# Kernel tuning notes

Hardware: AMD Instinct MI355X
Metric: run time of the kernel (lower is better)

Reference implementation:

```python
import jax, jax.numpy as jnp
from jax import lax
import numpy as np

B, DIM, H, W = 4, 64, 256, 256
HEADS = 8
# (pad_h, pad_w) for kernels (1,7),(1,11),(1,21),(7,1),(11,1),(21,1)
PADS = [(0, 3), (0, 5), (0, 10), (3, 0), (5, 0), (10, 0)]
KSHAPES = [(1, 7), (1, 11), (1, 21), (7, 1), (11, 1), (21, 1)]


def _ln(x, w, b):
    # LayerNorm over channel dim per pixel (torch does it in 'b (h w) c' layout)
    mu = jnp.mean(x, axis=1, keepdims=True)
    var = jnp.mean((x - mu) ** 2, axis=1, keepdims=True)  # unbiased=False
    return (x - mu) / jnp.sqrt(var + 1e-5) * w[None, :, None, None] + b[None, :, None, None]


def _dw(x, k, b, pad):
    # depthwise conv, k: (dim, 1, kh, kw)
    y = lax.conv_general_dilated(
        x, k, window_strides=(1, 1),
        padding=[(pad[0], pad[0]), (pad[1], pad[1])],
        feature_group_count=k.shape[0],
        dimension_numbers=('NCHW', 'OIHW', 'NCHW'))
    return y + b[None, :, None, None]


def _pw(x, w, b):
    # 1x1 conv
    return jnp.einsum('oc,bchw->bohw', w, x) + b[None, :, None, None]


def _l2n(x):
    # torch F.normalize(dim=-1): x / max(||x||_2, 1e-12)
    n = jnp.sqrt(jnp.sum(x * x, axis=-1, keepdims=True))
    return x / jnp.maximum(n, 1e-12)


def _to_attn(t, b, h, w, cph):
    # 'b (head c) h w -> b head w (h c)'  (h slow, c fast in last dim)
    t = t.reshape(b, HEADS, cph, h, w)
    return t.transpose(0, 1, 4, 3, 2).reshape(b, HEADS, w, h * cph)


def setup_inputs() -> dict:
    key = jax.random.key(0)
    keys = jax.random.split(key, 16)
    inp = {
        'x1': jax.random.normal(keys[0], (B, DIM, H, W), jnp.float32),
        'x2': jax.random.normal(keys[1], (B, DIM, H, W), jnp.float32),
        'ln1_w': jnp.ones((DIM,), jnp.float32),
        'ln1_b': jnp.zeros((DIM,), jnp.float32),
        'ln2_w': jnp.ones((DIM,), jnp.float32),
        'ln2_b': jnp.zeros((DIM,), jnp.float32),
        'b_dw': jnp.zeros((12, DIM), jnp.float32),
        'w_pw': 0.05 * jax.random.normal(keys[2], (DIM, DIM), jnp.float32),
        'b_pw': jnp.zeros((DIM,), jnp.float32),
    }
    names = ['k11', 'k12', 'k13', 'k14', 'k15', 'k16',
             'k21', 'k22', 'k23', 'k24', 'k25', 'k26']
    for i, nm in enumerate(names):
        kh, kw = KSHAPES[i % 6]
        inp[nm] = 0.1 * jax.random.normal(keys[3 + i], (DIM, 1, kh, kw), jnp.float32)
    return inp


def reference(x1, x2, ln1_w, ln1_b, ln2_w, ln2_b,
              k11, k12, k13, k14, k15, k16,
              k21, k22, k23, k24, k25, k26,
              b_dw, w_pw, b_pw):
    b, c, h, w = x2.shape
    cph = c // HEADS
    x1n = _ln(x1, ln1_w, ln1_b)
    x2n = _ln(x2, ln2_w, ln2_b)
    ks1 = (k11, k12, k13, k14, k15, k16)
    ks2 = (k21, k22, k23, k24, k25, k26)
    out1 = sum(_dw(x1n, k, b_dw[i], PADS[i]) for i, k in enumerate(ks1))
    out2 = sum(_dw(x2n, k, b_dw[6 + i], PADS[i]) for i, k in enumerate(ks2))
    out1 = _pw(out1, w_pw, b_pw)  # shared 1x1 conv (same weights for both)
    out2 = _pw(out2, w_pw, b_pw)
    q = _l2n(_to_attn(out1, b, h, w, cph))   # (b, head, w, h*cph)
    kk = _l2n(_to_attn(out2, b, h, w, cph))
    v = _to_attn(out2, b, h, w, cph)
    attn = jax.nn.softmax(jnp.einsum('bnwd,bnvd->bnwv', q, kk), axis=-1)
    out4 = jnp.einsum('bnwv,bnvd->bnwd', attn, v) + q
    out4 = out4.reshape(b, HEADS, w, h, cph).transpose(0, 1, 4, 3, 2).reshape(b, c, h, w)
    # note: torch rebinds x1/x2 to normalized tensors before the residual add
    return _pw(out4, w_pw, b_pw) + x1n + x2n
```

## Files before the change

kernel.cpp:

```cpp
#include <hip/hip_runtime.h>

#define HW 65536

typedef __bf16 bf16x8 __attribute__((ext_vector_type(8)));
typedef float f32x4 __attribute__((ext_vector_type(4)));

__device__ __forceinline__ float b2f(unsigned short u) {
    return __uint_as_float(((unsigned)u) << 16);
}
__device__ __forceinline__ unsigned short f2bu(float f) {
    unsigned u = __float_as_uint(f);
    return (unsigned short)((u + 0x7FFFu + ((u >> 16) & 1u)) >> 16);
}
__device__ __forceinline__ void up2(unsigned u, float& lo, float& hi) {
    lo = __uint_as_float(u << 16);
    hi = __uint_as_float(u & 0xFFFF0000u);
}

__global__ void k_prep(const float* k11, const float* k12, const float* k13,
                       const float* k14, const float* k15, const float* k16,
                       const float* k21, const float* k22, const float* k23,
                       const float* k24, const float* k25, const float* k26,
                       const float* bdw, float* wcomb, float* bias) {
    int c = threadIdx.x;
    if (c >= 64) return;
    float* wh1 = wcomb;
    float* wv1 = wcomb + 1344;
    float* wh2 = wcomb + 2688;
    float* wv2 = wcomb + 4032;
    for (int j = 0; j < 21; j++) {
        wh1[c*21+j] = k13[c*21+j];
        wv1[c*21+j] = k16[c*21+j];
        wh2[c*21+j] = k23[c*21+j];
        wv2[c*21+j] = k26[c*21+j];
    }
    for (int j = 0; j < 11; j++) {
        wh1[c*21+j+5] += k12[c*11+j];
        wv1[c*21+j+5] += k15[c*11+j];
        wh2[c*21+j+5] += k22[c*11+j];
        wv2[c*21+j+5] += k25[c*11+j];
    }
    for (int j = 0; j < 7; j++) {
        wh1[c*21+j+7] += k11[c*7+j];
        wv1[c*21+j+7] += k14[c*7+j];
        wh2[c*21+j+7] += k21[c*7+j];
        wv2[c*21+j+7] += k24[c*7+j];
    }
    float s1 = 0.f, s2 = 0.f;
    for (int i = 0; i < 6; i++) { s1 += bdw[i*64+c]; s2 += bdw[(6+i)*64+c]; }
    bias[c] = s1; bias[64+c] = s2;
}

__global__ __launch_bounds__(256) void k_ln(
        const float* __restrict__ x1, const float* __restrict__ x2,
        const float* __restrict__ w1, const float* __restrict__ b1,
        const float* __restrict__ w2, const float* __restrict__ b2,
        unsigned short* __restrict__ o1, unsigned short* __restrict__ o2,
        unsigned short* __restrict__ s12) {
    int p = blockIdx.x * 256 + threadIdx.x;
    int b = p >> 16, hw = p & (HW - 1);
    size_t base = (size_t)b * 64 * HW + hw;
    float v[64];
    unsigned n1[32];
    {
        float s = 0.f;
        #pragma unroll
        for (int c = 0; c < 64; c++) { v[c] = x1[base + (size_t)c * HW]; s += v[c]; }
        float mu = s * 0.015625f, s2 = 0.f;
        #pragma unroll
        for (int c = 0; c < 64; c++) { float d = v[c] - mu; s2 += d * d; }
        float rstd = rsqrtf(s2 * 0.015625f + 1e-5f);
        #pragma unroll
        for (int c2 = 0; c2 < 32; c2++) {
            unsigned short lo = f2bu((v[2*c2]   - mu) * rstd * w1[2*c2]   + b1[2*c2]);
            unsigned short hi = f2bu((v[2*c2+1] - mu) * rstd * w1[2*c2+1] + b1[2*c2+1]);
            o1[base + (size_t)(2*c2)   * HW] = lo;
            o1[base + (size_t)(2*c2+1) * HW] = hi;
            n1[c2] = (unsigned)lo | ((unsigned)hi << 16);
        }
    }
    {
        float s = 0.f;
        #pragma unroll
        for (int c = 0; c < 64; c++) { v[c] = x2[base + (size_t)c * HW]; s += v[c]; }
        float mu = s * 0.015625f, s2 = 0.f;
        #pragma unroll
        for (int c = 0; c < 64; c++) { float d = v[c] - mu; s2 += d * d; }
        float rstd = rsqrtf(s2 * 0.015625f + 1e-5f);
        #pragma unroll
        for (int c2 = 0; c2 < 32; c2++) {
            float a2 = (v[2*c2]   - mu) * rstd * w2[2*c2]   + b2[2*c2];
            float b2n = (v[2*c2+1] - mu) * rstd * w2[2*c2+1] + b2[2*c2+1];
            o2[base + (size_t)(2*c2)   * HW] = f2bu(a2);
            o2[base + (size_t)(2*c2+1) * HW] = f2bu(b2n);
            float lo, hi;
            up2(n1[c2], lo, hi);
            s12[base + (size_t)(2*c2)   * HW] = f2bu(lo + a2);
            s12[base + (size_t)(2*c2+1) * HW] = f2bu(hi + b2n);
        }
    }
}

__global__ __launch_bounds__(256) void k_dw(
        const unsigned short* __restrict__ in1, const unsigned short* __restrict__ in2,
        const float* __restrict__ wcomb, const float* __restrict__ bias,
        unsigned short* __restrict__ o1, unsigned short* __restrict__ o2) {
    __shared__ __align__(16) unsigned short tileRaw[52 * 320];
    __shared__ __align__(16) unsigned short ThT[16][64];
    __shared__ __align__(16) unsigned short TvA[16][64];
    int which = blockIdx.y;
    const unsigned short* in = which ? in2 : in1;
    unsigned short* o = which ? o2 : o1;
    int bx = blockIdx.x;
    int bc = bx >> 3, tileid = bx & 7;
    int c = bc & 63;
    int h0 = tileid * 32;
    int tid = threadIdx.x;

    {
        const float* whp = wcomb + which * 2688 + c * 21;
        const float* wvp = whp + 1344;
        for (int i = tid; i < 2048; i += 256) {
            int mat = i >> 10;
            int idx = i & 1023;
            int n = idx >> 6, k = idx & 63;
            int j = k - n - 6;
            float v = (j >= 0 && j < 21) ? (mat ? wvp[j] : whp[j]) : 0.f;
            (mat ? &TvA[0][0] : &ThT[0][0])[idx] = f2bu(v);
        }
    }
    const unsigned short* src = in + (size_t)bc * HW;
    for (int idx = tid; idx < 52 * 40; idx += 256) {
        int row = idx / 40, u = idx - row * 40;
        int grow = h0 - 10 + row;
        uint4 val = make_uint4(0u, 0u, 0u, 0u);
        if ((unsigned)grow < 256u && u >= 2 && u < 34)
            val = *(const uint4*)(src + grow * 256 + (u - 2) * 8);
        *(uint4*)&tileRaw[row * 320 + ((u ^ ((row >> 1) & 7)) << 3)] = val;
    }
    float bs = bias[which * 64 + c];
    __syncthreads();

    int lane = tid & 63, wid = tid >> 6;
    int rA = lane & 15, g = lane >> 4, kf = g * 8;

    bf16x8 thB0 = *(const bf16x8*)&ThT[rA][kf];
    bf16x8 thB1 = *(const bf16x8*)&ThT[rA][32 + kf];
    bf16x8 tvA0 = *(const bf16x8*)&TvA[rA][kf];
    bf16x8 tvA1 = *(const bf16x8*)&TvA[rA][32 + kf];

    int ht = wid & 1, wgrp = wid >> 1;
    for (int t = 0; t < 8; t++) {
        int w0 = (wgrp * 8 + t) * 16;
        int ub = w0 >> 3;
        int hrow = ht * 16 + rA + 10;
        int xh = (hrow >> 1) & 7;
        bf16x8 ax0 = *(const bf16x8*)&tileRaw[hrow * 320 + (((ub + g) ^ xh) << 3)];
        bf16x8 ax1 = *(const bf16x8*)&tileRaw[hrow * 320 + (((ub + 4 + g) ^ xh) << 3)];
        int uvb = ub + 2 + (rA >> 3);
        int el = rA & 7;
        uint4 bv0, bv1;
        unsigned* pv0 = (unsigned*)&bv0;
        unsigned* pv1 = (unsigned*)&bv1;
        #pragma unroll
        for (int e2 = 0; e2 < 4; e2++) {
            int k0i = kf + 2 * e2;
            int r0 = ht * 16 + k0i - 6;  r0 = r0 < 0 ? 0 : (r0 > 51 ? 51 : r0);
            int r1 = ht * 16 + k0i - 5;  r1 = r1 < 0 ? 0 : (r1 > 51 ? 51 : r1);
            unsigned lo = tileRaw[r0 * 320 + ((uvb ^ ((r0 >> 1) & 7)) << 3) + el];
            unsigned hi = tileRaw[r1 * 320 + ((uvb ^ ((r1 >> 1) & 7)) << 3) + el];
            pv0[e2] = lo | (hi << 16);
            int k1i = 32 + kf + 2 * e2;
            int r2 = ht * 16 + k1i - 6;  r2 = r2 < 0 ? 0 : (r2 > 51 ? 51 : r2);
            int r3 = ht * 16 + k1i - 5;  r3 = r3 < 0 ? 0 : (r3 > 51 ? 51 : r3);
            unsigned lo2 = tileRaw[r2 * 320 + ((uvb ^ ((r2 >> 1) & 7)) << 3) + el];
            unsigned hi2 = tileRaw[r3 * 320 + ((uvb ^ ((r3 >> 1) & 7)) << 3) + el];
            pv1[e2] = lo2 | (hi2 << 16);
        }
        f32x4 acc = {bs, bs, bs, bs};
        acc = __builtin_amdgcn_mfma_f32_16x16x32_bf16(ax0, thB0, acc, 0, 0, 0);
        acc = __builtin_amdgcn_mfma_f32_16x16x32_bf16(ax1, thB1, acc, 0, 0, 0);
        acc = __builtin_amdgcn_mfma_f32_16x16x32_bf16(tvA0, *(bf16x8*)&bv0, acc, 0, 0, 0);
        acc = __builtin_amdgcn_mfma_f32_16x16x32_bf16(tvA1, *(bf16x8*)&bv1, acc, 0, 0, 0);
        int wc = w0 + rA;
        size_t obase = (size_t)bc * HW + wc;
        #pragma unroll
        for (int r = 0; r < 4; r++) {
            int hh = h0 + ht * 16 + 4 * g + r;
            o[obase + (size_t)hh * 256] = f2bu(acc[r]);
        }
    }
}

__global__ __launch_bounds__(256) void k_pw(
        const unsigned short* __restrict__ in1, const unsigned short* __restrict__ in2,
        const float* __restrict__ wpw, const float* __restrict__ bpw,
        unsigned short* __restrict__ Eq, unsigned short* __restrict__ Fk,
        unsigned short* __restrict__ Fv) {
    __shared__ __align__(16) unsigned short Ws[64][72];
    __shared__ __align__(16) unsigned short Xs[64][260];
    __shared__ float sb[64];
    int tid = threadIdx.x;
    for (int i = tid; i < 4096; i += 256) Ws[i >> 6][i & 63] = f2bu(wpw[i]);
    if (tid < 64) sb[tid] = bpw[tid];
    int which = blockIdx.y;
    const unsigned short* in = which ? in2 : in1;
    int bx = blockIdx.x;
    int b = bx & 3;
    int h = ((bx >> 2) & 31) * 8 + (bx >> 7);
    const unsigned short* src = in + (size_t)b * 64 * HW + h * 256;
    for (int i = tid; i < 2048; i += 256) {
        int c = i >> 5, ch = i & 31;
        uint4 u = *(const uint4*)(src + (size_t)c * HW + ch * 8);
        *(uint2*)&Xs[c][ch * 8]     = make_uint2(u.x, u.y);
        *(uint2*)&Xs[c][ch * 8 + 4] = make_uint2(u.z, u.w);
    }
    __syncthreads();

    int lane = tid & 63, wv = tid >> 6;
    int rA = lane & 15, g = lane >> 4;
    int p_off = wv * 64;

    f32x4 acc[4][4];
    #pragma unroll
    for (int m = 0; m < 4; m++)
        #pragma unroll
        for (int n = 0; n < 4; n++) acc[m][n] = (f32x4){0.f, 0.f, 0.f, 0.f};

    #pragma unroll
    for (int ks = 0; ks < 2; ks++) {
        int c0 = ks * 32;
        bf16x8 a[4], bb[4];
        #pragma unroll
        for (int m = 0; m < 4; m++)
            a[m] = *(const bf16x8*)&Ws[16 * m + rA][c0 + 8 * g];
        #pragma unroll
        for (int n = 0; n < 4; n++) {
            int p = p_off + 16 * n + rA;
            uint4 bu;
            bu.x = (unsigned)Xs[c0 + 8*g + 0][p] | ((unsigned)Xs[c0 + 8*g + 1][p] << 16);
            bu.y = (unsigned)Xs[c0 + 8*g + 2][p] | ((unsigned)Xs[c0 + 8*g + 3][p] << 16);
            bu.z = (unsigned)Xs[c0 + 8*g + 4][p] | ((unsigned)Xs[c0 + 8*g + 5][p] << 16);
            bu.w = (unsigned)Xs[c0 + 8*g + 6][p] | ((unsigned)Xs[c0 + 8*g + 7][p] << 16);
            bb[n] = *(bf16x8*)&bu;
        }
        #pragma unroll
        for (int m = 0; m < 4; m++)
            #pragma unroll
            for (int n = 0; n < 4; n++)
                acc[m][n] = __builtin_amdgcn_mfma_f32_16x16x32_bf16(a[m], bb[n], acc[m][n], 0, 0, 0);
    }

    unsigned short* dst = which ? Fk : Eq;
    size_t b8 = (size_t)b * 8;
    #pragma unroll
    for (int m = 0; m < 4; m++) {
        int o0 = 16 * m + 4 * g;
        int hd = o0 >> 3, cp = o0 & 7;
        #pragma unroll
        for (int n = 0; n < 4; n++) {
            int p = p_off + 16 * n + rA;
            ushort4 pk;
            #pragma unroll
            for (int r = 0; r < 4; r++)
                ((unsigned short*)&pk)[r] = f2bu(acc[m][n][r] + sb[o0 + r]);
            *(ushort4*)(dst + ((b8 + hd) * 256 + p) * 2048 + h * 8 + cp) = pk;
            if (which) {
                #pragma unroll
                for (int r = 0; r < 4; r++) {
                    int o = o0 + r;
                    Fv[((b8 + (o >> 3)) * 2048 + h * 8 + (o & 7)) * 256 + p] =
                        ((unsigned short*)&pk)[r];
                }
            }
        }
    }
}

__global__ __launch_bounds__(256) void k_norm(
        const unsigned short* __restrict__ Eq, const unsigned short* __restrict__ Fk,
        float* __restrict__ invQ, float* __restrict__ invK) {
    int lane = threadIdx.x & 63, wid = threadIdx.x >> 6;
    int row = blockIdx.x * 4 + wid;
    const unsigned short* src = (row < 8192) ? Eq : Fk;
    int r = row & 8191;
    const unsigned short* p = src + (size_t)r * 2048;
    float s = 0.f;
    #pragma unroll
    for (int it = 0; it < 4; it++) {
        uint4 u = *(const uint4*)(p + it * 512 + lane * 8);
        unsigned vals[4] = {u.x, u.y, u.z, u.w};
        #pragma unroll
        for (int e = 0; e < 4; e++) {
            float lo = b2f((unsigned short)(vals[e] & 0xffffu));
            float hi = b2f((unsigned short)(vals[e] >> 16));
            s += lo * lo + hi * hi;
        }
    }
    #pragma unroll
    for (int m = 1; m < 64; m <<= 1) s += __shfl_xor(s, m, 64);
    if (lane == 0) {
        float inv = 1.f / fmaxf(sqrtf(s), 1e-12f);
        (row < 8192 ? invQ : invK)[r] = inv;
    }
}

__global__ __launch_bounds__(512, 4) void k_qkt(
        const unsigned short* __restrict__ Eq, const unsigned short* __restrict__ Fk,
        float* __restrict__ Sp) {
    int bx = blockIdx.x;
    int bh = bx & 31, t2 = bx >> 5;
    int itile = t2 >> 1, ks = t2 & 1;
    int i0 = itile * 32;
    const unsigned short* Q  = Eq + (size_t)bh * 524288 + ks * 1024;
    const unsigned short* Kp = Fk + (size_t)bh * 524288 + ks * 1024;
    int tid = threadIdx.x, lane = tid & 63, wid = tid >> 6;
    int rA = lane & 15, g = lane >> 4, kf = g * 8;

    f32x4 acc[2][2];
    #pragma unroll
    for (int ib = 0; ib < 2; ib++)
        #pragma unroll
        for (int jb = 0; jb < 2; jb++) acc[ib][jb] = (f32x4){0.f, 0.f, 0.f, 0.f};

    const unsigned short* q0  = Q  + (size_t)(i0 + rA) * 2048 + kf;
    const unsigned short* q1  = q0 + 16 * 2048;
    const unsigned short* kr0 = Kp + (size_t)(wid * 32 + rA) * 2048 + kf;
    const unsigned short* kr1 = kr0 + 16 * 2048;
    for (int k0 = 0; k0 < 1024; k0 += 128) {
        bf16x8 a0[4], a1[4], b0[4], b1[4];
        #pragma unroll
        for (int s = 0; s < 4; s++) {
            int kk = k0 + s * 32;
            a0[s] = *(const bf16x8*)(q0 + kk);
            a1[s] = *(const bf16x8*)(q1 + kk);
            b0[s] = *(const bf16x8*)(kr0 + kk);
            b1[s] = *(const bf16x8*)(kr1 + kk);
        }
        #pragma unroll
        for (int s = 0; s < 4; s++) {
            acc[0][0] = __builtin_amdgcn_mfma_f32_16x16x32_bf16(a0[s], b0[s], acc[0][0], 0, 0, 0);
            acc[1][0] = __builtin_amdgcn_mfma_f32_16x16x32_bf16(a1[s], b0[s], acc[1][0], 0, 0, 0);
            acc[0][1] = __builtin_amdgcn_mfma_f32_16x16x32_bf16(a0[s], b1[s], acc[0][1], 0, 0, 0);
            acc[1][1] = __builtin_amdgcn_mfma_f32_16x16x32_bf16(a1[s], b1[s], acc[1][1], 0, 0, 0);
        }
    }
    float* Sb = Sp + (size_t)(ks * 32 + bh) * 65536 + (size_t)i0 * 256;
    #pragma unroll
    for (int ib = 0; ib < 2; ib++)
        #pragma unroll
        for (int jb = 0; jb < 2; jb++)
            #pragma unroll
            for (int r = 0; r < 4; r++)
                Sb[(ib * 16 + g * 4 + r) * 256 + wid * 32 + jb * 16 + rA] = acc[ib][jb][r];
}

__global__ __launch_bounds__(256) void k_smx(
        const float* __restrict__ Sp, const float* __restrict__ invQ,
        const float* __restrict__ invK, unsigned short* __restrict__ P) {
    __shared__ float sKv[256];
    int bx = blockIdx.x;
    int bh = bx & 31, rg = bx >> 5;
    int tid = threadIdx.x;
    sKv[tid] = invK[bh * 256 + tid];
    __syncthreads();
    int lr = tid >> 5, sub = tid & 31;
    int i = rg * 8 + lr;
    int R = bh * 256 + i;
    const float* p0 = Sp + (size_t)bh * 65536 + i * 256;
    const float* p1 = Sp + (size_t)(32 + bh) * 65536 + i * 256;
    float qs = invQ[R];
    int c0 = sub * 8;
    float4 a0 = *(const float4*)(p0 + c0), a1 = *(const float4*)(p0 + c0 + 4);
    float4 b0 = *(const float4*)(p1 + c0), b1 = *(const float4*)(p1 + c0 + 4);
    float v[8];
    v[0] = (a0.x + b0.x); v[1] = (a0.y + b0.y); v[2] = (a0.z + b0.z); v[3] = (a0.w + b0.w);
    v[4] = (a1.x + b1.x); v[5] = (a1.y + b1.y); v[6] = (a1.z + b1.z); v[7] = (a1.w + b1.w);
    float m = -1e30f;
    #pragma unroll
    for (int e = 0; e < 8; e++) {
        v[e] *= qs * sKv[c0 + e];
        m = fmaxf(m, v[e]);
    }
    #pragma unroll
    for (int msk = 1; msk < 32; msk <<= 1) m = fmaxf(m, __shfl_xor(m, msk, 32));
    float s = 0.f;
    #pragma unroll
    for (int e = 0; e < 8; e++) { v[e] = __expf(v[e] - m); s += v[e]; }
    #pragma unroll
    for (int msk = 1; msk < 32; msk <<= 1) s += __shfl_xor(s, msk, 32);
    float inv = 1.f / s;
    uint4 w;
    w.x = (unsigned)f2bu(v[0] * inv) | ((unsigned)f2bu(v[1] * inv) << 16);
    w.y = (unsigned)f2bu(v[2] * inv) | ((unsigned)f2bu(v[3] * inv) << 16);
    w.z = (unsigned)f2bu(v[4] * inv) | ((unsigned)f2bu(v[5] * inv) << 16);
    w.w = (unsigned)f2bu(v[6] * inv) | ((unsigned)f2bu(v[7] * inv) << 16);
    *(uint4*)(P + (size_t)R * 256 + c0) = w;
}

__global__ __launch_bounds__(512, 4) void k_pv(
        const unsigned short* __restrict__ P, const unsigned short* __restrict__ Fv,
        const unsigned short* __restrict__ Eq, const float* __restrict__ invQ,
        unsigned short* __restrict__ G) {
    __shared__ __align__(16) unsigned short Pb[32][256];
    __shared__ __align__(16) unsigned short Qs[32][1024];
    __shared__ float sQ[32];
    int bx = blockIdx.x;
    int bh = bx & 31, t2 = bx >> 5;
    int itile = t2 >> 1, ds = t2 & 1;
    int i0 = itile * 32;
    int b = bh >> 3, hd = bh & 7;
    const unsigned short* Vt = Fv + (size_t)bh * 524288;
    int tid = threadIdx.x, lane = tid & 63, wid = tid >> 6;
    for (int i = tid; i < 1024; i += 512) {
        int r = i >> 5, cu = i & 31;
        uint4 u = *(const uint4*)(P + (size_t)(bh * 256 + i0 + r) * 256 + cu * 8);
        int su = cu ^ (r & 7);
        *(uint4*)&Pb[r][su * 8] = u;
    }
    for (int i = tid; i < 4096; i += 512) {
        int r = i >> 7, cu = i & 127;
        *(uint4*)&Qs[r][cu * 8] =
            *(const uint4*)(Eq + (size_t)(bh * 256 + i0 + r) * 2048 + ds * 1024 + cu * 8);
    }
    if (tid < 32) sQ[tid] = invQ[bh * 256 + i0 + tid];
    __syncthreads();

    int rA = lane & 15, g = lane >> 4, kf = g * 8;

    bf16x8 pa[2][8];
    #pragma unroll
    for (int ib = 0; ib < 2; ib++)
        #pragma unroll
        for (int ksl = 0; ksl < 8; ksl++) {
            int rr = ib * 16 + rA;
            int unit = (ksl * 4 + g) ^ (rr & 7);
            pa[ib][ksl] = *(const bf16x8*)&Pb[rr][unit * 8];
        }

    int dloc = wid * 128;
    for (int dt = 0; dt < 8; dt++) {
        int dl = dloc + dt * 16;
        int d0 = ds * 1024 + dl;
        const unsigned short* vp = Vt + (size_t)(d0 + rA) * 256 + kf;
        bf16x8 vb[8];
        #pragma unroll
        for (int ksl = 0; ksl < 8; ksl++)
            vb[ksl] = *(const bf16x8*)(vp + ksl * 32);
        f32x4 o0 = {0.f, 0.f, 0.f, 0.f}, o1 = {0.f, 0.f, 0.f, 0.f};
        #pragma unroll
        for (int ksl = 0; ksl < 8; ksl++) {
            o0 = __builtin_amdgcn_mfma_f32_16x16x32_bf16(pa[0][ksl], vb[ksl], o0, 0, 0, 0);
            o1 = __builtin_amdgcn_mfma_f32_16x16x32_bf16(pa[1][ksl], vb[ksl], o1, 0, 0, 0);
        }
        int d = d0 + rA;
        int dlr = dl + rA;
        int cpr = d & 7, hh = d >> 3;
        #pragma unroll
        for (int ib = 0; ib < 2; ib++) {
            f32x4 oa = ib ? o1 : o0;
            int ibase = i0 + ib * 16 + g * 4;
            ushort4 pk;
            #pragma unroll
            for (int r = 0; r < 4; r++) {
                int il = ib * 16 + g * 4 + r;
                float qv = b2f(Qs[il][dlr]) * sQ[il];
                ((unsigned short*)&pk)[r] = f2bu(oa[r] + qv);
            }
            *(ushort4*)(G + (size_t)(b * 64 + hd * 8 + cpr) * HW + hh * 256 + ibase) = pk;
        }
    }
}

__global__ __launch_bounds__(256) void k_final(
        const unsigned short* __restrict__ G, const unsigned short* __restrict__ S12g,
        const float* __restrict__ wpw, const float* __restrict__ bpw,
        float* __restrict__ out) {
    __shared__ __align__(16) unsigned short Ws[64][72];
    __shared__ __align__(16) unsigned short Gs[64][260];
    __shared__ __align__(16) unsigned short S12[64][260];
    __shared__ float sb[64];
    int tid = threadIdx.x;
    for (int i = tid; i < 4096; i += 256) Ws[i >> 6][i & 63] = f2bu(wpw[i]);
    if (tid < 64) sb[tid] = bpw[tid];
    int bx = blockIdx.x, b = bx >> 8, h = bx & 255;
    const unsigned short* src = G + (size_t)b * 64 * HW + h * 256;
    const unsigned short* ssrc = S12g + (size_t)b * 64 * HW + h * 256;
    for (int i = tid; i < 2048; i += 256) {
        int c = i >> 5, ch = i & 31;
        uint4 u = *(const uint4*)(src + (size_t)c * HW + ch * 8);
        *(uint2*)&Gs[c][ch * 8]     = make_uint2(u.x, u.y);
        *(uint2*)&Gs[c][ch * 8 + 4] = make_uint2(u.z, u.w);
        uint4 v = *(const uint4*)(ssrc + (size_t)c * HW + ch * 8);
        *(uint2*)&S12[c][ch * 8]     = make_uint2(v.x, v.y);
        *(uint2*)&S12[c][ch * 8 + 4] = make_uint2(v.z, v.w);
    }
    __syncthreads();

    int lane = tid & 63, wv = tid >> 6;
    int rA = lane & 15, g = lane >> 4;
    int p_off = wv * 64;

    f32x4 acc[4][4];
    #pragma unroll
    for (int m = 0; m < 4; m++)
        #pragma unroll
        for (int n = 0; n < 4; n++) acc[m][n] = (f32x4){0.f, 0.f, 0.f, 0.f};

    #pragma unroll
    for (int ks = 0; ks < 2; ks++) {
        int c0 = ks * 32;
        bf16x8 a[4], bb[4];
        #pragma unroll
        for (int m = 0; m < 4; m++)
            a[m] = *(const bf16x8*)&Ws[16 * m + rA][c0 + 8 * g];
        #pragma unroll
        for (int n = 0; n < 4; n++) {
            int p = p_off + 16 * n + rA;
            uint4 bu;
            bu.x = (unsigned)Gs[c0 + 8*g + 0][p] | ((unsigned)Gs[c0 + 8*g + 1][p] << 16);
            bu.y = (unsigned)Gs[c0 + 8*g + 2][p] | ((unsigned)Gs[c0 + 8*g + 3][p] << 16);
            bu.z = (unsigned)Gs[c0 + 8*g + 4][p] | ((unsigned)Gs[c0 + 8*g + 5][p] << 16);
            bu.w = (unsigned)Gs[c0 + 8*g + 6][p] | ((unsigned)Gs[c0 + 8*g + 7][p] << 16);
            bb[n] = *(bf16x8*)&bu;
        }
        #pragma unroll
        for (int m = 0; m < 4; m++)
            #pragma unroll
            for (int n = 0; n < 4; n++)
                acc[m][n] = __builtin_amdgcn_mfma_f32_16x16x32_bf16(a[m], bb[n], acc[m][n], 0, 0, 0);
    }

    #pragma unroll
    for (int m = 0; m < 4; m++) {
        int o0 = 16 * m + 4 * g;
        #pragma unroll
        for (int n = 0; n < 4; n++) {
            int p = p_off + 16 * n + rA;
            #pragma unroll
            for (int r = 0; r < 4; r++) {
                int o = o0 + r;
                out[(size_t)(b * 64 + o) * HW + h * 256 + p] =
                    acc[m][n][r] + sb[o] + b2f(S12[o][p]);
            }
        }
    }
}

extern "C" void kernel_launch(void* const* d_in, const int* in_sizes, int n_in,
                              void* d_out, int out_size, void* d_ws, size_t ws_size,
                              hipStream_t stream) {
    const float* x1   = (const float*)d_in[0];
    const float* x2   = (const float*)d_in[1];
    const float* ln1w = (const float*)d_in[2];
    const float* ln1b = (const float*)d_in[3];
    const float* ln2w = (const float*)d_in[4];
    const float* ln2b = (const float*)d_in[5];
    const float* bdw  = (const float*)d_in[6];
    const float* wpw  = (const float*)d_in[7];
    const float* bpw  = (const float*)d_in[8];
    const float* kk[12];
    for (int i = 0; i < 12; i++) kk[i] = (const float*)d_in[9 + i];

    char* ws = (char*)d_ws;
    float* wcomb = (float*)ws;
    float* bias  = (float*)(ws + 21504);
    float* invQ  = (float*)(ws + 32768);
    float* invK  = (float*)(ws + 65536);
    const size_t SMALL = 131072;
    const size_t SZ = 33554432;

    unsigned short* S12b = (unsigned short*)(ws + SMALL);
    unsigned short* S1 = (unsigned short*)(ws + SMALL + SZ);
    unsigned short* S2 = (unsigned short*)(ws + SMALL + 2 * SZ);
    unsigned short* S3 = (unsigned short*)(ws + SMALL + 3 * SZ);
    unsigned short* dw1 = (unsigned short*)d_out;
    unsigned short* dw2 = dw1 + SZ / 2;
    float* Sp = (float*)d_out;
    unsigned short* P = (unsigned short*)((char*)d_out + 20971520);

    k_prep<<<1, 64, 0, stream>>>(kk[0], kk[1], kk[2], kk[3], kk[4], kk[5],
                                 kk[6], kk[7], kk[8], kk[9], kk[10], kk[11],
                                 bdw, wcomb, bias);
    k_ln<<<1024, 256, 0, stream>>>(x1, x2, ln1w, ln1b, ln2w, ln2b, S1, S2, S12b);
    k_dw<<<dim3(2048, 2), 256, 0, stream>>>(S1, S2, wcomb, bias, dw1, dw2);
    k_pw<<<dim3(1024, 2), 256, 0, stream>>>(dw1, dw2, wpw, bpw, S1, S2, S3);
    k_norm<<<4096, 256, 0, stream>>>(S1, S2, invQ, invK);
    k_qkt<<<512, 512, 0, stream>>>(S1, S2, Sp);
    k_smx<<<1024, 256, 0, stream>>>(Sp, invQ, invK, P);
    k_pv<<<512, 512, 0, stream>>>(P, S3, S1, invQ, S2);
    k_final<<<1024, 256, 0, stream>>>(S2, S12b, wpw, bpw, (float*)d_out);
}
```

Measured before the change: 307.8 us.

## Stage QK^T tiles through swizzled LDS and tile V layout for coalesced MFMA loads

The QK^T kernel now cooperatively loads 64-wide K chunks for all 256 keys and the 32 query rows into XOR-swizzled shared memory, then feeds MFMA from LDS. Previously each wave fetched its own operands straight from global memory with strided per-lane loads. V is now written in a 16x8 blocked layout so that each lane's bf16x8 fragment in the PV kernel is one contiguous 16-byte chunk. The changes aim to cut redundant global traffic and uncoalesced access. In exchange they add two barriers per K chunk, about 36KB of LDS per block, and the occupancy hint is dropped.

```diff
diff --git a/kernel.cpp b/kernel.cpp
--- a/kernel.cpp
+++ b/kernel.cpp
@@ -269,8 +269,10 @@
                 #pragma unroll
                 for (int r = 0; r < 4; r++) {
                     int o = o0 + r;
-                    Fv[((b8 + (o >> 3)) * 2048 + h * 8 + (o & 7)) * 256 + p] =
-                        ((unsigned short*)&pk)[r];
+                    int d = h * 8 + (o & 7);
+                    size_t vbase = (b8 + (size_t)(o >> 3)) * 524288;
+                    int idx = (((d >> 4) * 32 + (p >> 3)) << 7) + ((d & 15) << 3) + (p & 7);
+                    Fv[vbase + idx] = ((unsigned short*)&pk)[r];
                 }
             }
         }
@@ -305,54 +307,59 @@
     }
 }
 
-__global__ __launch_bounds__(512, 4) void k_qkt(
+__global__ __launch_bounds__(512) void k_qkt(
         const unsigned short* __restrict__ Eq, const unsigned short* __restrict__ Fk,
         float* __restrict__ Sp) {
+    __shared__ __align__(16) unsigned short KsRaw[256 * 64];
+    __shared__ __align__(16) unsigned short QsRaw[32 * 64];
     int bx = blockIdx.x;
     int bh = bx & 31, t2 = bx >> 5;
     int itile = t2 >> 1, ks = t2 & 1;
     int i0 = itile * 32;
-    const unsigned short* Q  = Eq + (size_t)bh * 524288 + ks * 1024;
-    const unsigned short* Kp = Fk + (size_t)bh * 524288 + ks * 1024;
+    const unsigned short* Qb = Eq + (size_t)bh * 524288 + ks * 1024;
+    const unsigned short* Kb = Fk + (size_t)bh * 524288 + ks * 1024;
     int tid = threadIdx.x, lane = tid & 63, wid = tid >> 6;
-    int rA = lane & 15, g = lane >> 4, kf = g * 8;
-
-    f32x4 acc[2][2];
-    #pragma unroll
-    for (int ib = 0; ib < 2; ib++)
-        #pragma unroll
-        for (int jb = 0; jb < 2; jb++) acc[ib][jb] = (f32x4){0.f, 0.f, 0.f, 0.f};
-
-    const unsigned short* q0  = Q  + (size_t)(i0 + rA) * 2048 + kf;
-    const unsigned short* q1  = q0 + 16 * 2048;
-    const unsigned short* kr0 = Kp + (size_t)(wid * 32 + rA) * 2048 + kf;
-    const unsigned short* kr1 = kr0 + 16 * 2048;
-    for (int k0 = 0; k0 < 1024; k0 += 128) {
-        bf16x8 a0[4], a1[4], b0[4], b1[4];
-        #pragma unroll
-        for (int s = 0; s < 4; s++) {
-            int kk = k0 + s * 32;
-            a0[s] = *(const bf16x8*)(q0 + kk);
-            a1[s] = *(const bf16x8*)(q1 + kk);
-            b0[s] = *(const bf16x8*)(kr0 + kk);
-            b1[s] = *(const bf16x8*)(kr1 + kk);
-        }
-        #pragma unroll
-        for (int s = 0; s < 4; s++) {
-            acc[0][0] = __builtin_amdgcn_mfma_f32_16x16x32_bf16(a0[s], b0[s], acc[0][0], 0, 0, 0);
-            acc[1][0] = __builtin_amdgcn_mfma_f32_16x16x32_bf16(a1[s], b0[s], acc[1][0], 0, 0, 0);
-            acc[0][1] = __builtin_amdgcn_mfma_f32_16x16x32_bf16(a0[s], b1[s], acc[0][1], 0, 0, 0);
-            acc[1][1] = __builtin_amdgcn_mfma_f32_16x16x32_bf16(a1[s], b1[s], acc[1][1], 0, 0, 0);
-        }
+    int rA = lane & 15, g = lane >> 4;
+    int rt = wid & 1, cg = wid >> 1;
+
+    f32x4 acc[4];
+    #pragma unroll
+    for (int n = 0; n < 4; n++) acc[n] = (f32x4){0.f, 0.f, 0.f, 0.f};
+
+    for (int kc = 0; kc < 1024; kc += 64) {
+        #pragma unroll
+        for (int it = 0; it < 4; it++) {
+            int idx = it * 512 + tid;
+            int row = idx >> 3, c8 = idx & 7;
+            *(uint4*)&KsRaw[row * 64 + ((c8 ^ (row & 7)) << 3)] =
+                *(const uint4*)(Kb + (size_t)row * 2048 + kc + c8 * 8);
+        }
+        if (tid < 256) {
+            int row = tid >> 3, c8 = tid & 7;
+            *(uint4*)&QsRaw[row * 64 + ((c8 ^ (row & 7)) << 3)] =
+                *(const uint4*)(Qb + (size_t)(i0 + row) * 2048 + kc + c8 * 8);
+        }
+        __syncthreads();
+        #pragma unroll
+        for (int kk = 0; kk < 2; kk++) {
+            int c8 = kk * 4 + g;
+            int arow = rt * 16 + rA;
+            bf16x8 a = *(const bf16x8*)&QsRaw[arow * 64 + ((c8 ^ (arow & 7)) << 3)];
+            #pragma unroll
+            for (int n = 0; n < 4; n++) {
+                int brow = cg * 64 + n * 16 + rA;
+                bf16x8 b = *(const bf16x8*)&KsRaw[brow * 64 + ((c8 ^ (brow & 7)) << 3)];
+                acc[n] = __builtin_amdgcn_mfma_f32_16x16x32_bf16(a, b, acc[n], 0, 0, 0);
+            }
+        }
+        __syncthreads();
     }
     float* Sb = Sp + (size_t)(ks * 32 + bh) * 65536 + (size_t)i0 * 256;
     #pragma unroll
-    for (int ib = 0; ib < 2; ib++)
-        #pragma unroll
-        for (int jb = 0; jb < 2; jb++)
-            #pragma unroll
-            for (int r = 0; r < 4; r++)
-                Sb[(ib * 16 + g * 4 + r) * 256 + wid * 32 + jb * 16 + rA] = acc[ib][jb][r];
+    for (int n = 0; n < 4; n++)
+        #pragma unroll
+        for (int r = 0; r < 4; r++)
+            Sb[(rt * 16 + g * 4 + r) * 256 + cg * 64 + n * 16 + rA] = acc[n][r];
 }
 
 __global__ __launch_bounds__(256) void k_smx(
@@ -426,7 +433,7 @@
     if (tid < 32) sQ[tid] = invQ[bh * 256 + i0 + tid];
     __syncthreads();
 
-    int rA = lane & 15, g = lane >> 4, kf = g * 8;
+    int rA = lane & 15, g = lane >> 4;
 
     bf16x8 pa[2][8];
     #pragma unroll
@@ -442,11 +449,11 @@
     for (int dt = 0; dt < 8; dt++) {
         int dl = dloc + dt * 16;
         int d0 = ds * 1024 + dl;
-        const unsigned short* vp = Vt + (size_t)(d0 + rA) * 256 + kf;
+        int D = d0 >> 4;
         bf16x8 vb[8];
         #pragma unroll
         for (int ksl = 0; ksl < 8; ksl++)
-            vb[ksl] = *(const bf16x8*)(vp + ksl * 32);
+            vb[ksl] = *(const bf16x8*)&Vt[(size_t)(D * 32 + ksl * 4 + g) * 128 + rA * 8];
         f32x4 o0 = {0.f, 0.f, 0.f, 0.f}, o1 = {0.f, 0.f, 0.f, 0.f};
         #pragma unroll
         for (int ksl = 0; ksl < 8; ksl++) {
```

Result: faster. 263.6 us (-14.4%).
